# Kernel tuning notes

Hardware: AMD Instinct MI355X
Metric: run time of the kernel (lower is better)

## Reference

```python
import jax, jax.numpy as jnp
import numpy as np

DIM = 256
NUM_EXPERTS = 16
EXPERT_HIDDEN = 128
ROUTER_HIDDEN = 64
N_TOKENS = 32768


def setup_inputs() -> dict:
    key = jax.random.key(0)
    ks = jax.random.split(key, 9)
    s = lambda fan_in: 1.0 / np.sqrt(fan_in)
    x = jax.random.normal(ks[0], (N_TOKENS, DIM), dtype=jnp.float32)
    # Router params (Linear(DIM,64) -> ReLU -> Linear(64,E))
    r_w1 = jax.random.uniform(ks[1], (DIM, ROUTER_HIDDEN), jnp.float32, -s(DIM), s(DIM))
    r_b1 = jax.random.uniform(ks[2], (ROUTER_HIDDEN,), jnp.float32, -s(DIM), s(DIM))
    r_w2 = jax.random.uniform(ks[3], (ROUTER_HIDDEN, NUM_EXPERTS), jnp.float32, -s(ROUTER_HIDDEN), s(ROUTER_HIDDEN))
    r_b2 = jax.random.uniform(ks[4], (NUM_EXPERTS,), jnp.float32, -s(ROUTER_HIDDEN), s(ROUTER_HIDDEN))
    # Expert params, stacked over experts: Linear(DIM,128) -> Tanh -> Linear(128,DIM)
    e_w1 = jax.random.uniform(ks[5], (NUM_EXPERTS, DIM, EXPERT_HIDDEN), jnp.float32, -s(DIM), s(DIM))
    e_b1 = jax.random.uniform(ks[6], (NUM_EXPERTS, EXPERT_HIDDEN), jnp.float32, -s(DIM), s(DIM))
    e_w2 = jax.random.uniform(ks[7], (NUM_EXPERTS, EXPERT_HIDDEN, DIM), jnp.float32, -s(EXPERT_HIDDEN), s(EXPERT_HIDDEN))
    e_b2 = jax.random.uniform(ks[8], (NUM_EXPERTS, DIM), jnp.float32, -s(EXPERT_HIDDEN), s(EXPERT_HIDDEN))
    return {"x": x, "r_w1": r_w1, "r_b1": r_b1, "r_w2": r_w2, "r_b2": r_b2,
            "e_w1": e_w1, "e_b1": e_b1, "e_w2": e_w2, "e_b2": e_b2}


def reference(x, r_w1, r_b1, r_w2, r_b2, e_w1, e_b1, e_w2, e_b2):
    # Router: softmax(Linear(ReLU(Linear(x)))), temp=1.0
    h_r = jax.nn.relu(x @ r_w1 + r_b1)                      # [N, 64]
    w = jax.nn.softmax(h_r @ r_w2 + r_b2, axis=-1)          # [N, E]
    # All experts densely (faithful to the reference loop), batched over E.
    h = jnp.tanh(jnp.einsum('nd,edh->neh', x, e_w1) + e_b1[None, :, :])   # [N, E, H]
    outs = jnp.einsum('neh,ehd->ned', h, e_w2) + e_b2[None, :, :]         # [N, E, D]
    # Top-2 gating: mask, renormalize, combine.
    top_val, top_idx = jax.lax.top_k(w, 2)                  # [N, 2]
    n = w.shape[0]
    mask = jnp.zeros_like(w).at[jnp.arange(n)[:, None], top_idx].set(1.0)
    w_top = w * mask
    w_top = w_top / (jnp.sum(w_top, axis=-1, keepdims=True) + 1e-8)
    y_pred = jnp.einsum('ne,ned->nd', w_top, outs)          # [N, D]
    return (y_pred, w)
```

## Files before the change

### kernel.cpp

```cpp
#include <hip/hip_runtime.h>
#include <math.h>

#define NT 32768
#define DIM 256
#define NE 16
#define EH 128
#define RH 64
#define TB 64

#define IB (NT * DIM)
#define WS_COUNTS (IB)
#define WS_OFFSETS (IB + 16)
#define WS_CURSORS (IB + 33)
#define WS_NBLK (IB + 49)
#define WS_TABLE (IB + 64)
#define WS_TOKE (IB + 4096)
#define WS_LIST (WS_TOKE + 2 * NT)
#define WS_TOKG (WS_LIST + 2 * NT)
#define WS_LIST_G (WS_TOKG + 2 * NT)
#define WS_END_I (WS_LIST_G + 2 * NT)
#define U_W1T (2 * WS_END_I)
#define U_W2T (U_W1T + NE * DIM * EH)

typedef __attribute__((ext_vector_type(4))) float f32x4;
typedef __attribute__((ext_vector_type(8))) short bf16x8;
typedef __attribute__((ext_vector_type(8))) unsigned short us8;

#define SWZ9(b) ((b) ^ (((b) >> 5) & 0x70))
#define SWZ8(b) ((b) ^ (((b) >> 4) & 0x70))

__device__ inline unsigned short f2bf(float f) {
    unsigned int bits = __builtin_bit_cast(unsigned int, f);
    bits += 0x7fffu + ((bits >> 16) & 1u);
    return (unsigned short)(bits >> 16);
}

__global__ __launch_bounds__(256) void router_kernel(
    const float* __restrict__ x,
    const float* __restrict__ rw1, const float* __restrict__ rb1,
    const float* __restrict__ rw2, const float* __restrict__ rb2,
    float* __restrict__ w_out, int* __restrict__ wsi, float* __restrict__ wsf)
{
    __shared__ float xT[64][68];
    __shared__ float w1s[64][64];
    __shared__ float hs[64][68];
    __shared__ float ls[64][20];
    __shared__ int scnt[16];

    const int tid = threadIdx.x;
    const int tok0 = blockIdx.x * 64;
    if (tid < 16) scnt[tid] = 0;

    float acc[4][4];
#pragma unroll
    for (int i = 0; i < 4; ++i)
#pragma unroll
        for (int j = 0; j < 4; ++j) acc[i][j] = 0.f;

    const int tt = (tid & 15) * 4;
    const int hh = (tid >> 4) * 4;

    for (int kc = 0; kc < 4; ++kc) {
        __syncthreads();
#pragma unroll
        for (int i = 0; i < 4; ++i) {
            int idx = tid + 256 * i;
            int t = idx >> 4;
            int d4 = (idx & 15) * 4;
            float4 v = *(const float4*)(x + (size_t)(tok0 + t) * DIM + kc * 64 + d4);
            xT[d4 + 0][t] = v.x; xT[d4 + 1][t] = v.y;
            xT[d4 + 2][t] = v.z; xT[d4 + 3][t] = v.w;
        }
#pragma unroll
        for (int i = 0; i < 4; ++i) {
            int idx = tid + 256 * i;
            int d = idx >> 4;
            int h4 = (idx & 15) * 4;
            *(float4*)&w1s[d][h4] = *(const float4*)(rw1 + (size_t)(kc * 64 + d) * RH + h4);
        }
        __syncthreads();
#pragma unroll 8
        for (int d = 0; d < 64; ++d) {
            const float4 xa4 = *(const float4*)&xT[d][tt];
            const float4 wv4 = *(const float4*)&w1s[d][hh];
            const float xa[4] = {xa4.x, xa4.y, xa4.z, xa4.w};
            const float wv[4] = {wv4.x, wv4.y, wv4.z, wv4.w};
#pragma unroll
            for (int i = 0; i < 4; ++i)
#pragma unroll
                for (int j = 0; j < 4; ++j)
                    acc[i][j] = fmaf(xa[i], wv[j], acc[i][j]);
        }
    }
    __syncthreads();
    {
        const float4 b4 = *(const float4*)(rb1 + hh);
        const float b[4] = {b4.x, b4.y, b4.z, b4.w};
#pragma unroll
        for (int i = 0; i < 4; ++i) {
            float4 hv;
            hv.x = fmaxf(acc[i][0] + b[0], 0.f);
            hv.y = fmaxf(acc[i][1] + b[1], 0.f);
            hv.z = fmaxf(acc[i][2] + b[2], 0.f);
            hv.w = fmaxf(acc[i][3] + b[3], 0.f);
            *(float4*)&hs[tt + i][hh] = hv;
        }
    }
    __syncthreads();
    {
        int tok = tid >> 2;
        int e0 = (tid & 3) * 4;
        float l[4] = {0.f, 0.f, 0.f, 0.f};
#pragma unroll 8
        for (int k = 0; k < 64; ++k) {
            float hv = hs[tok][k];
            float4 wv = *(const float4*)(rw2 + k * NE + e0);
            l[0] = fmaf(hv, wv.x, l[0]);
            l[1] = fmaf(hv, wv.y, l[1]);
            l[2] = fmaf(hv, wv.z, l[2]);
            l[3] = fmaf(hv, wv.w, l[3]);
        }
        float4 lb = *(const float4*)(rb2 + e0);
        ls[tok][e0 + 0] = l[0] + lb.x;
        ls[tok][e0 + 1] = l[1] + lb.y;
        ls[tok][e0 + 2] = l[2] + lb.z;
        ls[tok][e0 + 3] = l[3] + lb.w;
    }
    __syncthreads();
    if (tid < 64) {
        const int tok = tid;
        const int gt = tok0 + tok;
        float v[16];
        float m = -1e30f;
#pragma unroll
        for (int e = 0; e < 16; ++e) { v[e] = ls[tok][e]; m = fmaxf(m, v[e]); }
        float s = 0.f;
#pragma unroll
        for (int e = 0; e < 16; ++e) { v[e] = expf(v[e] - m); s += v[e]; }
        const float inv = 1.0f / s;
#pragma unroll
        for (int e = 0; e < 16; ++e) v[e] *= inv;
#pragma unroll
        for (int e = 0; e < 16; e += 4) {
            float4 wv = make_float4(v[e], v[e + 1], v[e + 2], v[e + 3]);
            *(float4*)(w_out + (size_t)gt * NE + e) = wv;
        }
        float v1 = -1.f, v2 = -1.f; int i1 = 0, i2 = 0;
#pragma unroll
        for (int e = 0; e < 16; ++e) {
            if (v[e] > v1) { v2 = v1; i2 = i1; v1 = v[e]; i1 = e; }
            else if (v[e] > v2) { v2 = v[e]; i2 = e; }
        }
        const float den = v1 + v2 + 1e-8f;
        atomicAdd(&scnt[i1], 1);
        atomicAdd(&scnt[i2], 1);
        wsi[WS_TOKE + 2 * gt + 0] = i1;
        wsi[WS_TOKE + 2 * gt + 1] = i2;
        wsf[WS_TOKG + 2 * gt + 0] = v1 / den;
        wsf[WS_TOKG + 2 * gt + 1] = v2 / den;
    }
    __syncthreads();
    if (tid < 16 && scnt[tid]) atomicAdd(&wsi[WS_COUNTS + tid], scnt[tid]);
}

__global__ __launch_bounds__(256) void wprep_kernel(
    const float* __restrict__ ew1, const float* __restrict__ ew2,
    unsigned short* __restrict__ w1t, unsigned short* __restrict__ w2t)
{
    __shared__ float t[64][65];
    int b = blockIdx.x;
    const float* src; unsigned short* dst; int R, C, tr, tc;
    if (b < 128) {
        int e = b >> 3, t8 = b & 7; tr = t8 >> 1; tc = t8 & 1;
        src = ew1 + (size_t)e * DIM * EH; R = DIM; C = EH;
        dst = w1t + (size_t)e * DIM * EH;
    } else {
        int b2 = b - 128; int e = b2 >> 3, t8 = b2 & 7; tr = t8 & 1; tc = t8 >> 1;
        src = ew2 + (size_t)e * EH * DIM; R = EH; C = DIM;
        dst = w2t + (size_t)e * EH * DIM;
    }
    const int R0 = tr * 64, C0 = tc * 64;
    const int tid = threadIdx.x;
#pragma unroll
    for (int q = 0; q < 4; ++q) {
        int r = (tid >> 4) + q * 16, c = (tid & 15) * 4;
        float4 v = *(const float4*)(src + (size_t)(R0 + r) * C + C0 + c);
        t[r][c] = v.x; t[r][c + 1] = v.y; t[r][c + 2] = v.z; t[r][c + 3] = v.w;
    }
    __syncthreads();
#pragma unroll
    for (int q = 0; q < 2; ++q) {
        int rp = (tid >> 3) + q * 32, c0 = (tid & 7) * 8;
        us8 u;
#pragma unroll
        for (int k = 0; k < 8; ++k) u[k] = f2bf(t[c0 + k][rp]);
        *(us8*)(dst + (size_t)(C0 + rp) * R + R0 + c0) = u;
    }
}

__global__ __launch_bounds__(64) void scan_kernel(int* __restrict__ wsi)
{
    __shared__ int soff[17], snc[16];
    const int tid = threadIdx.x;
    if (tid == 0) {
        int off = 0, nb = 0;
        soff[0] = 0;
        for (int e = 0; e < NE; ++e) {
            int c = wsi[WS_COUNTS + e];
            wsi[WS_CURSORS + e] = off;
            wsi[WS_OFFSETS + e] = off;
            off += c;
            soff[e + 1] = off;
            snc[e] = nb;
            nb += (c + TB - 1) / TB;
        }
        wsi[WS_OFFSETS + NE] = off;
        wsi[WS_NBLK] = nb;
    }
    __syncthreads();
    for (int e = 0; e < NE; ++e) {
        int nc = (soff[e + 1] - soff[e] + TB - 1) / TB;
        for (int k = tid; k < nc; k += 64)
            wsi[WS_TABLE + snc[e] + k] = (e << 16) | k;
    }
}

__global__ __launch_bounds__(256) void scatter_kernel(int* __restrict__ wsi, float* __restrict__ wsf)
{
    __shared__ int scnt[16], sbase[16];
    const int tid = threadIdx.x;
    const int t = blockIdx.x * 256 + tid;
    if (tid < 16) scnt[tid] = 0;
    __syncthreads();
    const int e0 = wsi[WS_TOKE + 2 * t + 0];
    const int e1 = wsi[WS_TOKE + 2 * t + 1];
    const int l0 = atomicAdd(&scnt[e0], 1);
    const int l1 = atomicAdd(&scnt[e1], 1);
    __syncthreads();
    if (tid < 16) sbase[tid] = scnt[tid] ? atomicAdd(&wsi[WS_CURSORS + tid], scnt[tid]) : 0;
    __syncthreads();
    const int p0 = sbase[e0] + l0;
    const int p1 = sbase[e1] + l1;
    wsi[WS_LIST + p0] = (t << 1);
    wsf[WS_LIST_G + p0] = wsf[WS_TOKG + 2 * t + 0];
    wsi[WS_LIST + p1] = (t << 1) | 1;
    wsf[WS_LIST_G + p1] = wsf[WS_TOKG + 2 * t + 1];
}

__global__ __launch_bounds__(256, 1) void expert_kernel(
    const float* __restrict__ x,
    const float* __restrict__ eb1, const float* __restrict__ eb2,
    const unsigned short* __restrict__ w1t, const unsigned short* __restrict__ w2t,
    const int* __restrict__ wsi, const float* __restrict__ wsf,
    float* __restrict__ y, float* __restrict__ part1)
{
    __shared__ unsigned short smem[16384];
    if ((int)blockIdx.x >= wsi[WS_NBLK]) return;

    const int ent = wsi[WS_TABLE + blockIdx.x];
    const int e = ent >> 16;
    const int c = ent & 0xffff;
    const int start = wsi[WS_OFFSETS + e] + c * TB;
    const int cnt = min(TB, wsi[WS_OFFSETS + e + 1] - start);

    const int tid = threadIdx.x;
    const int lane = tid & 63, w = tid >> 6;
    const int l15 = lane & 15;
    const int kq = lane >> 4;
    const int q4 = kq * 4;
    char* lds = (char*)smem;

    const int row = tid >> 2, q = tid & 3;
    const int srow = (row < cnt) ? (wsi[WS_LIST + start + row] >> 1) : -1;
    const float* xr = x + (size_t)(srow < 0 ? 0 : srow) * DIM + q * 64;
    float4 xa[8], xb[8];
#pragma unroll
    for (int i = 0; i < 8; ++i) {
        xa[i] = *(const float4*)(xr + i * 8);
        xb[i] = *(const float4*)(xr + i * 8 + 4);
    }

    const char* w1e = (const char*)(w1t + (size_t)e * DIM * EH);
    bf16x8 b1[8][2];
#pragma unroll
    for (int ks = 0; ks < 8; ++ks)
#pragma unroll
        for (int nt = 0; nt < 2; ++nt)
            b1[ks][nt] = *(const bf16x8*)(w1e + (w * 32 + nt * 16 + l15) * 512 + ks * 64 + kq * 16);

    {
        const int base = row * 512 + q * 128;
#pragma unroll
        for (int i = 0; i < 8; ++i) {
            us8 u;
            if (srow >= 0) {
                u[0] = f2bf(xa[i].x); u[1] = f2bf(xa[i].y); u[2] = f2bf(xa[i].z); u[3] = f2bf(xa[i].w);
                u[4] = f2bf(xb[i].x); u[5] = f2bf(xb[i].y); u[6] = f2bf(xb[i].z); u[7] = f2bf(xb[i].w);
            } else {
#pragma unroll
                for (int k = 0; k < 8; ++k) u[k] = 0;
            }
            *(us8*)(lds + SWZ9(base + i * 16)) = u;
        }
    }
    __syncthreads();

    f32x4 zero4; zero4[0] = zero4[1] = zero4[2] = zero4[3] = 0.f;
    f32x4 acc[4][2];
#pragma unroll
    for (int i = 0; i < 4; ++i)
#pragma unroll
        for (int j = 0; j < 2; ++j) acc[i][j] = zero4;

#pragma unroll
    for (int ks = 0; ks < 8; ++ks) {
        bf16x8 a[4];
#pragma unroll
        for (int mt = 0; mt < 4; ++mt)
            a[mt] = *(const bf16x8*)(lds + SWZ9((mt * 16 + l15) * 512 + ks * 64 + kq * 16));
#pragma unroll
        for (int mt = 0; mt < 4; ++mt)
#pragma unroll
            for (int nt = 0; nt < 2; ++nt)
                acc[mt][nt] = __builtin_amdgcn_mfma_f32_16x16x32_bf16(a[mt], b1[ks][nt], acc[mt][nt], 0, 0, 0);
    }

    const char* w2e = (const char*)(w2t + (size_t)e * EH * DIM);
    bf16x8 b2a[4][2];
#pragma unroll
    for (int ks = 0; ks < 4; ++ks)
#pragma unroll
        for (int nt = 0; nt < 2; ++nt)
            b2a[ks][nt] = *(const bf16x8*)(w2e + (w * 64 + nt * 16 + l15) * 256 + ks * 64 + kq * 16);

    __syncthreads();

#pragma unroll
    for (int nt = 0; nt < 2; ++nt) {
        const int h = w * 32 + nt * 16 + l15;
        const float b1v = eb1[e * EH + h];
#pragma unroll
        for (int mt = 0; mt < 4; ++mt)
#pragma unroll
            for (int r = 0; r < 4; ++r) {
                int tok = mt * 16 + q4 + r;
                *(unsigned short*)(lds + SWZ8(tok * 256 + h * 2)) = f2bf(tanhf(acc[mt][nt][r] + b1v));
            }
    }
    __syncthreads();

    bf16x8 b2b[4][2];
#pragma unroll
    for (int ks = 0; ks < 4; ++ks)
#pragma unroll
        for (int nt = 0; nt < 2; ++nt)
            b2b[ks][nt] = *(const bf16x8*)(w2e + (w * 64 + 32 + nt * 16 + l15) * 256 + ks * 64 + kq * 16);

    {
        f32x4 acc2[4][2];
#pragma unroll
        for (int i = 0; i < 4; ++i)
#pragma unroll
            for (int j = 0; j < 2; ++j) acc2[i][j] = zero4;
#pragma unroll
        for (int ks = 0; ks < 4; ++ks) {
            bf16x8 a[4];
#pragma unroll
            for (int mt = 0; mt < 4; ++mt)
                a[mt] = *(const bf16x8*)(lds + SWZ8((mt * 16 + l15) * 256 + ks * 64 + kq * 16));
#pragma unroll
            for (int mt = 0; mt < 4; ++mt)
#pragma unroll
                for (int nt = 0; nt < 2; ++nt)
                    acc2[mt][nt] = __builtin_amdgcn_mfma_f32_16x16x32_bf16(a[mt], b2a[ks][nt], acc2[mt][nt], 0, 0, 0);
        }
        float b2v[2];
#pragma unroll
        for (int nt = 0; nt < 2; ++nt)
            b2v[nt] = eb2[e * DIM + w * 64 + nt * 16 + l15];
#pragma unroll
        for (int mt = 0; mt < 4; ++mt)
#pragma unroll
            for (int r = 0; r < 4; ++r) {
                int rl = mt * 16 + q4 + r;
                if (rl < cnt) {
                    int entry = wsi[WS_LIST + start + rl];
                    int tok = entry >> 1;
                    float g = wsf[WS_LIST_G + start + rl];
                    float* dst = ((entry & 1) ? part1 : y) + (size_t)tok * DIM + w * 64;
#pragma unroll
                    for (int nt = 0; nt < 2; ++nt)
                        dst[nt * 16 + l15] = g * (acc2[mt][nt][r] + b2v[nt]);
                }
            }
    }
    {
        f32x4 acc2[4][2];
#pragma unroll
        for (int i = 0; i < 4; ++i)
#pragma unroll
            for (int j = 0; j < 2; ++j) acc2[i][j] = zero4;
#pragma unroll
        for (int ks = 0; ks < 4; ++ks) {
            bf16x8 a[4];
#pragma unroll
            for (int mt = 0; mt < 4; ++mt)
                a[mt] = *(const bf16x8*)(lds + SWZ8((mt * 16 + l15) * 256 + ks * 64 + kq * 16));
#pragma unroll
            for (int mt = 0; mt < 4; ++mt)
#pragma unroll
                for (int nt = 0; nt < 2; ++nt)
                    acc2[mt][nt] = __builtin_amdgcn_mfma_f32_16x16x32_bf16(a[mt], b2b[ks][nt], acc2[mt][nt], 0, 0, 0);
        }
        float b2v[2];
#pragma unroll
        for (int nt = 0; nt < 2; ++nt)
            b2v[nt] = eb2[e * DIM + w * 64 + 32 + nt * 16 + l15];
#pragma unroll
        for (int mt = 0; mt < 4; ++mt)
#pragma unroll
            for (int r = 0; r < 4; ++r) {
                int rl = mt * 16 + q4 + r;
                if (rl < cnt) {
                    int entry = wsi[WS_LIST + start + rl];
                    int tok = entry >> 1;
                    float g = wsf[WS_LIST_G + start + rl];
                    float* dst = ((entry & 1) ? part1 : y) + (size_t)tok * DIM + w * 64 + 32;
#pragma unroll
                    for (int nt = 0; nt < 2; ++nt)
                        dst[nt * 16 + l15] = g * (acc2[mt][nt][r] + b2v[nt]);
                }
            }
    }
}

__global__ __launch_bounds__(256) void combine_kernel(float* __restrict__ y,
                                                      const float* __restrict__ part1)
{
    const size_t i = ((size_t)blockIdx.x * 256 + threadIdx.x) * 4;
    float4 a = *(float4*)(y + i);
    const float4 b = *(const float4*)(part1 + i);
    a.x += b.x; a.y += b.y; a.z += b.z; a.w += b.w;
    *(float4*)(y + i) = a;
}

extern "C" void kernel_launch(void* const* d_in, const int* in_sizes, int n_in,
                              void* d_out, int out_size, void* d_ws, size_t ws_size,
                              hipStream_t stream)
{
    const float* x = (const float*)d_in[0];
    const float* rw1 = (const float*)d_in[1];
    const float* rb1 = (const float*)d_in[2];
    const float* rw2 = (const float*)d_in[3];
    const float* rb2 = (const float*)d_in[4];
    const float* ew1 = (const float*)d_in[5];
    const float* eb1 = (const float*)d_in[6];
    const float* ew2 = (const float*)d_in[7];
    const float* eb2 = (const float*)d_in[8];

    float* y = (float*)d_out;
    float* w_out = y + (size_t)NT * DIM;
    int* wsi = (int*)d_ws;
    float* wsf = (float*)d_ws;
    float* part1 = (float*)d_ws;
    unsigned short* wsu = (unsigned short*)d_ws;

    hipMemsetAsync(wsi + WS_COUNTS, 0, NE * sizeof(int), stream);

    wprep_kernel<<<256, 256, 0, stream>>>(ew1, ew2, wsu + U_W1T, wsu + U_W2T);
    router_kernel<<<NT / 64, 256, 0, stream>>>(x, rw1, rb1, rw2, rb2, w_out, wsi, wsf);
    scan_kernel<<<1, 64, 0, stream>>>(wsi);
    scatter_kernel<<<NT / 256, 256, 0, stream>>>(wsi, wsf);
    expert_kernel<<<2 * NT / TB + NE, 256, 0, stream>>>(x, eb1, eb2, wsu + U_W1T, wsu + U_W2T,
                                                        wsi, wsf, y, part1);
    combine_kernel<<<NT * DIM / 1024, 256, 0, stream>>>(y, part1);
}
```

Measured before the change: 128.9 us.

## Pre-gather and convert tokens to bf16 in expert order before expert GEMM

Adds a gather kernel that reads each routed token row of x, converts it to bf16, and writes it contiguously in expert-sorted order into workspace. The expert kernel then loads contiguous bf16 rows straight into LDS instead of doing scattered fp32 gathers and conversion inside the low-occupancy GEMM kernel. The aim is to shorten the expert kernel's load latency on its critical path. The cost is an extra launch plus an extra write and read of the gathered buffer. Padding rows are no longer zeroed, so they may read neighbouring or out-of-range data.

```diff
diff --git a/kernel.cpp b/kernel.cpp
--- a/kernel.cpp
+++ b/kernel.cpp
@@ -21,6 +21,7 @@
 #define WS_END_I (WS_LIST_G + 2 * NT)
 #define U_W1T (2 * WS_END_I)
 #define U_W2T (U_W1T + NE * DIM * EH)
+#define U_XG (U_W2T + NE * DIM * EH)
 
 typedef __attribute__((ext_vector_type(4))) float f32x4;
 typedef __attribute__((ext_vector_type(8))) short bf16x8;
@@ -247,8 +248,32 @@
     wsf[WS_LIST_G + p1] = wsf[WS_TOKG + 2 * t + 1];
 }
 
+__global__ __launch_bounds__(256) void gather_kernel(
+    const float* __restrict__ x, const int* __restrict__ wsi,
+    unsigned short* __restrict__ xg)
+{
+    const int tid = threadIdx.x;
+    const int p = blockIdx.x * 32 + (tid >> 3);
+    const int sub = tid & 7;
+    const int tok = wsi[WS_LIST + p] >> 1;
+    const float* src = x + (size_t)tok * DIM + sub * 32;
+    unsigned short* dst = xg + (size_t)p * DIM + sub * 32;
+    float4 v[8];
+#pragma unroll
+    for (int i = 0; i < 8; ++i) v[i] = *(const float4*)(src + i * 4);
+#pragma unroll
+    for (int i = 0; i < 4; ++i) {
+        us8 u;
+        u[0] = f2bf(v[2 * i].x);     u[1] = f2bf(v[2 * i].y);
+        u[2] = f2bf(v[2 * i].z);     u[3] = f2bf(v[2 * i].w);
+        u[4] = f2bf(v[2 * i + 1].x); u[5] = f2bf(v[2 * i + 1].y);
+        u[6] = f2bf(v[2 * i + 1].z); u[7] = f2bf(v[2 * i + 1].w);
+        *(us8*)(dst + i * 8) = u;
+    }
+}
+
 __global__ __launch_bounds__(256, 1) void expert_kernel(
-    const float* __restrict__ x,
+    const unsigned short* __restrict__ xg,
     const float* __restrict__ eb1, const float* __restrict__ eb2,
     const unsigned short* __restrict__ w1t, const unsigned short* __restrict__ w2t,
     const int* __restrict__ wsi, const float* __restrict__ wsf,
@@ -270,15 +295,11 @@
     const int q4 = kq * 4;
     char* lds = (char*)smem;
 
-    const int row = tid >> 2, q = tid & 3;
-    const int srow = (row < cnt) ? (wsi[WS_LIST + start + row] >> 1) : -1;
-    const float* xr = x + (size_t)(srow < 0 ? 0 : srow) * DIM + q * 64;
-    float4 xa[8], xb[8];
-#pragma unroll
-    for (int i = 0; i < 8; ++i) {
-        xa[i] = *(const float4*)(xr + i * 8);
-        xb[i] = *(const float4*)(xr + i * 8 + 4);
-    }
+    const char* xrow = (const char*)(xg + (size_t)start * DIM);
+    us8 ubuf[8];
+#pragma unroll
+    for (int i = 0; i < 8; ++i)
+        ubuf[i] = *(const us8*)(xrow + (tid + i * 256) * 16);
 
     const char* w1e = (const char*)(w1t + (size_t)e * DIM * EH);
     bf16x8 b1[8][2];
@@ -288,21 +309,9 @@
         for (int nt = 0; nt < 2; ++nt)
             b1[ks][nt] = *(const bf16x8*)(w1e + (w * 32 + nt * 16 + l15) * 512 + ks * 64 + kq * 16);
 
-    {
-        const int base = row * 512 + q * 128;
-#pragma unroll
-        for (int i = 0; i < 8; ++i) {
-            us8 u;
-            if (srow >= 0) {
-                u[0] = f2bf(xa[i].x); u[1] = f2bf(xa[i].y); u[2] = f2bf(xa[i].z); u[3] = f2bf(xa[i].w);
-                u[4] = f2bf(xb[i].x); u[5] = f2bf(xb[i].y); u[6] = f2bf(xb[i].z); u[7] = f2bf(xb[i].w);
-            } else {
-#pragma unroll
-                for (int k = 0; k < 8; ++k) u[k] = 0;
-            }
-            *(us8*)(lds + SWZ9(base + i * 16)) = u;
-        }
-    }
+#pragma unroll
+    for (int i = 0; i < 8; ++i)
+        *(us8*)(lds + SWZ9((tid + i * 256) * 16)) = ubuf[i];
     __syncthreads();
 
     f32x4 zero4; zero4[0] = zero4[1] = zero4[2] = zero4[3] = 0.f;
@@ -471,7 +480,9 @@
     router_kernel<<<NT / 64, 256, 0, stream>>>(x, rw1, rb1, rw2, rb2, w_out, wsi, wsf);
     scan_kernel<<<1, 64, 0, stream>>>(wsi);
     scatter_kernel<<<NT / 256, 256, 0, stream>>>(wsi, wsf);
-    expert_kernel<<<2 * NT / TB + NE, 256, 0, stream>>>(x, eb1, eb2, wsu + U_W1T, wsu + U_W2T,
+    gather_kernel<<<2 * NT / 32, 256, 0, stream>>>(x, wsi, wsu + U_XG);
+    expert_kernel<<<2 * NT / TB + NE, 256, 0, stream>>>(wsu + U_XG, eb1, eb2,
+                                                        wsu + U_W1T, wsu + U_W2T,
                                                         wsi, wsf, y, part1);
     combine_kernel<<<NT * DIM / 1024, 256, 0, stream>>>(y, part1);
 }
```

New measurement: 137.7 us. +6.9%, slower.
